# Kernel optimization log

Hardware: AMD Instinct MI355X
Metric: run time of the kernel (lower is better)

The kernel has to match this reference:

```python
import jax, jax.numpy as jnp
import numpy as np

NUM_HEADS = 8
EPS = 1e-6


def setup_inputs() -> dict:
    key = jax.random.key(0)
    k1, k2, k3 = jax.random.split(key, 3)
    B, N, C = 4, 256, 512
    x = jax.random.normal(k1, (B, N, C), dtype=jnp.float32)
    w_qkv = jax.random.normal(k2, (3 * C, C), dtype=jnp.float32) * (C ** -0.5)
    w_proj = jax.random.normal(k3, (C, C), dtype=jnp.float32) * (C ** -0.5)
    b_proj = jnp.zeros((C,), dtype=jnp.float32)
    paramR = jnp.ones((1,), dtype=jnp.float32)
    return {"x": x, "w_qkv": w_qkv, "w_proj": w_proj, "b_proj": b_proj, "paramR": paramR}


def _fourier_attention(x, w_qkv, w_proj, b_proj, paramR):
    B, N, C = x.shape
    H = NUM_HEADS
    Dh = C // H
    # qkv projection (no bias), split into per-head q,k,v: (B,H,N,Dh)
    qkv = jnp.einsum('bnc,kc->bnk', x, w_qkv).reshape(B, N, 3, H, Dh)
    q = qkv[:, :, 0].transpose(0, 2, 1, 3)
    k = qkv[:, :, 1].transpose(0, 2, 1, 3)
    v = qkv[:, :, 2].transpose(0, 2, 1, 3)
    R = paramR[0]
    # Generalized Fourier integral kernel: prod_d sin(R*(q_d - k_d))/(q_d - k_d)
    diff = q[:, :, :, None, :] - k[:, :, None, :, :]  # (B,H,Nq,Nk,Dh)
    near0 = jnp.abs(diff) < 1e-8
    safe = jnp.where(near0, jnp.float32(1.0), diff)
    s = jnp.where(near0, R, jnp.sin(R * safe) / safe)
    score = jnp.prod(s, axis=-1)  # (B,H,Nq,Nk)
    a4 = score ** 4
    attn = a4 / (jnp.sum(a4, axis=-1, keepdims=True) + EPS)  # normalize over keys
    out = jnp.einsum('bhqk,bhkd->bhqd', attn, v)
    out = out.transpose(0, 2, 1, 3).reshape(B, N, C)
    return jnp.einsum('bnc,oc->bno', out, w_proj) + b_proj


def reference(x, w_qkv, w_proj, b_proj, paramR):
    return _fourier_attention(x, w_qkv, w_proj, b_proj, paramR)
```

## Files before the change

kernel.cpp:

```cpp
#include <hip/hip_runtime.h>
#include <math.h>

#define BB 4
#define NN 256
#define CC 512
#define HH 8
#define DH 64

typedef __attribute__((ext_vector_type(8))) short bf16x8;
typedef __attribute__((ext_vector_type(4))) float f32x4;
typedef __attribute__((ext_vector_type(2))) float f32x2;

__device__ inline unsigned short f2bf(float f) {
  unsigned u = __float_as_uint(f);
  u += 0x7FFFu + ((u >> 16) & 1u);
  return (unsigned short)(u >> 16);
}
__device__ inline float bf2f(unsigned short s) {
  return __uint_as_float((unsigned)s << 16);
}

__global__ __launch_bounds__(256) void cvt_hilo3(
    const float* __restrict__ in0, unsigned short* __restrict__ h0,
    unsigned short* __restrict__ l0, const float* __restrict__ in1,
    unsigned short* __restrict__ h1, unsigned short* __restrict__ l1,
    const float* __restrict__ in2, unsigned short* __restrict__ h2,
    unsigned short* __restrict__ l2) {
  int b = blockIdx.x;
  const float* in;
  unsigned short *h, *l;
  if (b < 512) {
    in = in0; h = h0; l = l0;
  } else if (b < 1280) {
    in = in1; h = h1; l = l1; b -= 512;
  } else {
    in = in2; h = h2; l = l2; b -= 1280;
  }
  int i = (b * 256 + threadIdx.x) * 4;
  float4 f = *(const float4*)(in + i);
  float fa[4] = {f.x, f.y, f.z, f.w};
  ushort4 hv, lv;
  unsigned short* hp = (unsigned short*)&hv;
  unsigned short* lp = (unsigned short*)&lv;
#pragma unroll
  for (int j = 0; j < 4; j++) {
    unsigned short hb = f2bf(fa[j]);
    hp[j] = hb;
    lp[j] = f2bf(fa[j] - bf2f(hb));
  }
  *(ushort4*)(h + i) = hv;
  *(ushort4*)(l + i) = lv;
}

template <bool BIAS>
__global__ __launch_bounds__(256, 2) void gemm_mfma(
    const unsigned short* __restrict__ Ah, const unsigned short* __restrict__ Al,
    const unsigned short* __restrict__ Bh, const unsigned short* __restrict__ Bl,
    const float* __restrict__ bias, float* __restrict__ C, int M, int N,
    int K) {
  __shared__ unsigned short sAh[2][64][72], sAl[2][64][72];
  __shared__ unsigned short sBh[2][64][72], sBl[2][64][72];
  const int t = threadIdx.x;
  const int lane = t & 63;
  const int w = t >> 6;
  const int bm = blockIdx.y * 64;
  const int bn = blockIdx.x * 64;
  const int wr = (w >> 1) * 32;
  const int wc = (w & 1) * 32;
  const int quad = lane >> 4;
  const int l16 = lane & 15;

  const int r0 = t >> 3;
  const int r1 = r0 + 32;
  const int c8 = (t & 7) * 8;

  const size_t a0 = (size_t)(bm + r0) * K + c8;
  const size_t a1 = (size_t)(bm + r1) * K + c8;
  const size_t b0 = (size_t)(bn + r0) * K + c8;
  const size_t b1 = (size_t)(bn + r1) * K + c8;

  f32x4 acc[2][2];
#pragma unroll
  for (int i = 0; i < 2; i++)
#pragma unroll
    for (int j = 0; j < 2; j++) {
      acc[i][j][0] = 0.f;
      acc[i][j][1] = 0.f;
      acc[i][j][2] = 0.f;
      acc[i][j][3] = 0.f;
    }

  uint4 pa0, pa1, pa2, pa3, pb0, pb1, pb2, pb3;
#define GLOADS(K0)                       \
  pa0 = *(const uint4*)(Ah + a0 + (K0)); \
  pa1 = *(const uint4*)(Ah + a1 + (K0)); \
  pa2 = *(const uint4*)(Al + a0 + (K0)); \
  pa3 = *(const uint4*)(Al + a1 + (K0)); \
  pb0 = *(const uint4*)(Bh + b0 + (K0)); \
  pb1 = *(const uint4*)(Bh + b1 + (K0)); \
  pb2 = *(const uint4*)(Bl + b0 + (K0)); \
  pb3 = *(const uint4*)(Bl + b1 + (K0));

#define STORE(P)                  \
  *(uint4*)&sAh[P][r0][c8] = pa0; \
  *(uint4*)&sAh[P][r1][c8] = pa1; \
  *(uint4*)&sAl[P][r0][c8] = pa2; \
  *(uint4*)&sAl[P][r1][c8] = pa3; \
  *(uint4*)&sBh[P][r0][c8] = pb0; \
  *(uint4*)&sBh[P][r1][c8] = pb1; \
  *(uint4*)&sBl[P][r0][c8] = pb2; \
  *(uint4*)&sBl[P][r1][c8] = pb3;

  GLOADS(0)
  STORE(0)
  __syncthreads();
  GLOADS(64)

  int p = 0;
  for (int k0 = 0; k0 < K; k0 += 64) {
#pragma unroll
    for (int kk = 0; kk < 2; kk++) {
      const int kc = kk * 32 + quad * 8;
      bf16x8 ah[2], al[2], bh[2], bl[2];
#pragma unroll
      for (int i = 0; i < 2; i++) {
        ah[i] = *(const bf16x8*)&sAh[p][wr + i * 16 + l16][kc];
        al[i] = *(const bf16x8*)&sAl[p][wr + i * 16 + l16][kc];
        bh[i] = *(const bf16x8*)&sBh[p][wc + i * 16 + l16][kc];
        bl[i] = *(const bf16x8*)&sBl[p][wc + i * 16 + l16][kc];
      }
#pragma unroll
      for (int i = 0; i < 2; i++)
#pragma unroll
        for (int j = 0; j < 2; j++) {
          acc[i][j] = __builtin_amdgcn_mfma_f32_16x16x32_bf16(
              ah[i], bh[j], acc[i][j], 0, 0, 0);
          acc[i][j] = __builtin_amdgcn_mfma_f32_16x16x32_bf16(
              ah[i], bl[j], acc[i][j], 0, 0, 0);
          acc[i][j] = __builtin_amdgcn_mfma_f32_16x16x32_bf16(
              al[i], bh[j], acc[i][j], 0, 0, 0);
        }
    }
    if (k0 + 64 < K) {
      STORE(p ^ 1)
      if (k0 + 128 < K) {
        GLOADS(k0 + 128)
      }
    }
    __syncthreads();
    p ^= 1;
  }
#undef GLOADS
#undef STORE

#pragma unroll
  for (int i = 0; i < 2; i++)
#pragma unroll
    for (int j = 0; j < 2; j++) {
      int n = bn + wc + j * 16 + l16;
      float bv = BIAS ? bias[n] : 0.f;
#pragma unroll
      for (int r = 0; r < 4; r++) {
        int m = bm + wr + i * 16 + quad * 4 + r;
        C[(size_t)m * N + n] = acc[i][j][r] + bv;
      }
    }
}

__global__ __launch_bounds__(512) void fourier_attn(
    const float* __restrict__ qkv, const float* __restrict__ paramR,
    float* __restrict__ num0, float* __restrict__ num1,
    float* __restrict__ den0, float* __restrict__ den1) {
  __shared__ float Kt[64][68];
  __shared__ float Qs[16][64];
  __shared__ unsigned short Pah[16][72];
  __shared__ unsigned short Pal[16][72];
  __shared__ f32x4 Red[4][64];

  const int t = threadIdx.x;
  const int lane = t & 63;
  const int wv = t >> 6;
  const int quad = lane >> 4;
  const int l16 = lane & 15;
  const int h = blockIdx.x & 7;
  const int b = blockIdx.x >> 3;
  const int qc = blockIdx.y >> 1;
  const int kc = blockIdx.y & 1;
  const float R = paramR[0];
  const float cR = R * 0.15915494309189535f;

  const float* base = qkv + (size_t)b * NN * (3 * CC) + h * DH;

  if (t < 256) {
    int r = t >> 4;
    int c4 = (t & 15) << 2;
    *(float4*)&Qs[r][c4] =
        *(const float4*)(base + (size_t)(qc * 16 + r) * (3 * CC) + c4);
  }

  const int qi0 = wv * 2, qi1 = wv * 2 + 1;
  float Sp[2] = {0.f, 0.f};
  f32x4 oacc;
  oacc[0] = 0.f; oacc[1] = 0.f; oacc[2] = 0.f; oacc[3] = 0.f;

  const int nc = wv & 3;
  const int g2 = wv >> 2;
  const int kb = g2 * 32 + quad * 8;
  const int vcol = nc * 16 + l16;

  float4 pk[2];
#define LOADK(JT)                                                          \
  _Pragma("unroll") for (int u0 = 0; u0 < 2; u0++) {                       \
    int u = t + 512 * u0;                                                  \
    int r_ = u >> 4;                                                       \
    int c4_ = (u & 15) << 2;                                               \
    pk[u0] =                                                               \
        *(const float4*)(base + (size_t)((JT) * 64 + r_) * (3 * CC) + CC + \
                         c4_);                                             \
  }

  LOADK(kc * 2)

  const f32x2 eps2 = {1e-30f, 1e-30f};
  const f32x2 cR2 = {cR, cR};

  for (int jj = 0; jj < 2; jj++) {
    const int jt = kc * 2 + jj;
    __syncthreads();
#pragma unroll
    for (int u0 = 0; u0 < 2; u0++) {
      int u = t + 512 * u0;
      int r = u >> 4;
      int c4 = (u & 15) << 2;
      *(float4*)&Kt[r][c4] = pk[u0];
    }
    __syncthreads();
    if (jj == 0) {
      LOADK(kc * 2 + 1)
    }

    f32x2 nmA0 = {1.f, 1.f}, nmB0 = {1.f, 1.f};
    f32x2 nmA1 = {1.f, 1.f}, nmB1 = {1.f, 1.f};
    f32x2 dnA0 = {1.f, 1.f}, dnB0 = {1.f, 1.f};
    f32x2 dnA1 = {1.f, 1.f}, dnB1 = {1.f, 1.f};
#pragma unroll
    for (int d4 = 0; d4 < 16; d4++) {
      float4 k4 = *(const float4*)&Kt[lane][4 * d4];
      float4 qa = *(const float4*)&Qs[qi0][4 * d4];
      float4 qb = *(const float4*)&Qs[qi1][4 * d4];
      f32x2 kA = {k4.x, k4.y};
      f32x2 kB = {k4.z, k4.w};
      f32x2 dA0 = ((f32x2){qa.x, qa.y} - kA) + eps2;
      f32x2 dB0 = ((f32x2){qa.z, qa.w} - kB) + eps2;
      f32x2 dA1 = ((f32x2){qb.x, qb.y} - kA) + eps2;
      f32x2 dB1 = ((f32x2){qb.z, qb.w} - kB) + eps2;
      f32x2 gA0 = cR2 * dA0, gB0 = cR2 * dB0;
      f32x2 gA1 = cR2 * dA1, gB1 = cR2 * dB1;
      f32x2 sA0, sB0, sA1, sB1;
      sA0.x = __builtin_amdgcn_sinf(gA0.x);
      sA0.y = __builtin_amdgcn_sinf(gA0.y);
      sB0.x = __builtin_amdgcn_sinf(gB0.x);
      sB0.y = __builtin_amdgcn_sinf(gB0.y);
      sA1.x = __builtin_amdgcn_sinf(gA1.x);
      sA1.y = __builtin_amdgcn_sinf(gA1.y);
      sB1.x = __builtin_amdgcn_sinf(gB1.x);
      sB1.y = __builtin_amdgcn_sinf(gB1.y);
      nmA0 *= sA0;
      nmB0 *= sB0;
      nmA1 *= sA1;
      nmB1 *= sB1;
      dnA0 *= dA0;
      dnB0 *= dB0;
      dnA1 *= dA1;
      dnB1 *= dB1;
    }

    float vf[8];
#pragma unroll
    for (int j = 0; j < 8; j++) {
      vf[j] = base[(size_t)(jt * 64 + kb + j) * (3 * CC) + 2 * CC + vcol];
    }

    {
      f32x2 n0 = nmA0 * nmB0, d0 = dnA0 * dnB0;
      f32x2 n1 = nmA1 * nmB1, d1 = dnA1 * dnB1;
      float sc0 = (n0.x * n0.y) / (d0.x * d0.y);
      float sc1 = (n1.x * n1.y) / (d1.x * d1.y);
      float t0 = sc0 * sc0, t1 = sc1 * sc1;
      float a40 = t0 * t0, a41 = t1 * t1;
      Sp[0] += a40;
      Sp[1] += a41;
      unsigned short h0 = f2bf(a40), h1 = f2bf(a41);
      Pah[qi0][lane] = h0;
      Pal[qi0][lane] = f2bf(a40 - bf2f(h0));
      Pah[qi1][lane] = h1;
      Pal[qi1][lane] = f2bf(a41 - bf2f(h1));
    }
    __syncthreads();

    {
      bf16x8 pah = *(const bf16x8*)&Pah[l16][kb];
      bf16x8 pal = *(const bf16x8*)&Pal[l16][kb];
      bf16x8 vh, vl;
#pragma unroll
      for (int j = 0; j < 8; j++) {
        float f = vf[j];
        unsigned short hb = f2bf(f);
        vh[j] = (short)hb;
        vl[j] = (short)f2bf(f - bf2f(hb));
      }
      __builtin_amdgcn_s_setprio(1);
      oacc = __builtin_amdgcn_mfma_f32_16x16x32_bf16(pah, vh, oacc, 0, 0, 0);
      oacc = __builtin_amdgcn_mfma_f32_16x16x32_bf16(pah, vl, oacc, 0, 0, 0);
      oacc = __builtin_amdgcn_mfma_f32_16x16x32_bf16(pal, vh, oacc, 0, 0, 0);
      __builtin_amdgcn_s_setprio(0);
    }
  }
#undef LOADK

  float* nump = kc ? num1 : num0;
  float* denp = kc ? den1 : den0;
#pragma unroll
  for (int q = 0; q < 2; q++) {
    float s = Sp[q];
#pragma unroll
    for (int off = 32; off > 0; off >>= 1) s += __shfl_xor(s, off, 64);
    if (lane == 0) {
      int m = b * NN + qc * 16 + qi0 + q;
      denp[(size_t)m * HH + h] = s;
    }
  }
  if (wv >= 4) Red[wv - 4][lane] = oacc;
  __syncthreads();
  if (wv < 4) {
    f32x4 part = Red[wv][lane];
#pragma unroll
    for (int r = 0; r < 4; r++) {
      int q = quad * 4 + r;
      int m = b * NN + qc * 16 + q;
      nump[(size_t)m * CC + h * DH + nc * 16 + l16] = oacc[r] + part[r];
    }
  }
}

__global__ __launch_bounds__(256) void combine_norm(
    const float* __restrict__ num0, const float* __restrict__ num1,
    const float* __restrict__ den0, const float* __restrict__ den1,
    unsigned short* __restrict__ aoh, unsigned short* __restrict__ aol) {
  int e = (blockIdx.x * 256 + threadIdx.x) * 4;
  int m = e >> 9;
  int hd = (e >> 6) & 7;
  float den = den0[(size_t)m * HH + hd] + den1[(size_t)m * HH + hd] + 1e-6f;
  float4 n0 = *(const float4*)(num0 + e);
  float4 n1 = *(const float4*)(num1 + e);
  float o[4] = {(n0.x + n1.x) / den, (n0.y + n1.y) / den,
                (n0.z + n1.z) / den, (n0.w + n1.w) / den};
  ushort4 hv, lv;
  unsigned short* hp = (unsigned short*)&hv;
  unsigned short* lp = (unsigned short*)&lv;
#pragma unroll
  for (int j = 0; j < 4; j++) {
    unsigned short hb = f2bf(o[j]);
    hp[j] = hb;
    lp[j] = f2bf(o[j] - bf2f(hb));
  }
  *(ushort4*)(aoh + e) = hv;
  *(ushort4*)(aol + e) = lv;
}

extern "C" void kernel_launch(void* const* d_in, const int* in_sizes, int n_in,
                              void* d_out, int out_size, void* d_ws,
                              size_t ws_size, hipStream_t stream) {
  const float* x = (const float*)d_in[0];
  const float* w_qkv = (const float*)d_in[1];
  const float* w_proj = (const float*)d_in[2];
  const float* b_proj = (const float*)d_in[3];
  const float* paramR = (const float*)d_in[4];
  float* outp = (float*)d_out;

  const int nX = BB * NN * CC;
  const int nWq = 3 * CC * CC;
  const int nWp = CC * CC;

  unsigned short* xh = (unsigned short*)d_ws;
  unsigned short* xl = xh + nX;
  unsigned short* wqh = xl + nX;
  unsigned short* wql = wqh + nWq;
  unsigned short* wph = wql + nWq;
  unsigned short* wpl = wph + nWp;
  unsigned short* aoh = wpl + nWp;
  unsigned short* aol = aoh + nX;
  float* qkv_ws = (float*)(aol + nX);
  float* num0 = qkv_ws + 1024 * 1536;
  float* num1 = num0 + nX;
  float* den0 = num1 + nX;
  float* den1 = den0 + 1024 * HH;

  cvt_hilo3<<<1536, 256, 0, stream>>>(x, xh, xl, w_qkv, wqh, wql, w_proj, wph,
                                      wpl);

  gemm_mfma<false><<<dim3(3 * CC / 64, BB * NN / 64), 256, 0, stream>>>(
      xh, xl, wqh, wql, nullptr, qkv_ws, BB * NN, 3 * CC, CC);

  fourier_attn<<<dim3(HH * BB, (NN / 16) * 2), 512, 0, stream>>>(
      qkv_ws, paramR, num0, num1, den0, den1);

  combine_norm<<<nX / 1024, 256, 0, stream>>>(num0, num1, den0, den1, aoh,
                                              aol);

  gemm_mfma<true><<<dim3(CC / 64, BB * NN / 64), 256, 0, stream>>>(
      aoh, aol, wph, wpl, b_proj, outp, BB * NN, CC, CC);
}
```

Before: 128.5 us.

## Split attention into 4 key chunks with 8-query, 256-thread blocks

```diff
diff --git a/kernel.cpp b/kernel.cpp
--- a/kernel.cpp
+++ b/kernel.cpp
@@ -167,15 +167,16 @@
     }
 }
 
-__global__ __launch_bounds__(512) void fourier_attn(
+__global__ __launch_bounds__(256) void fourier_attn(
     const float* __restrict__ qkv, const float* __restrict__ paramR,
     float* __restrict__ num0, float* __restrict__ num1,
-    float* __restrict__ den0, float* __restrict__ den1) {
+    float* __restrict__ num2, float* __restrict__ num3,
+    float* __restrict__ den0, float* __restrict__ den1,
+    float* __restrict__ den2, float* __restrict__ den3) {
   __shared__ float Kt[64][68];
-  __shared__ float Qs[16][64];
+  __shared__ float Qs[8][64];
   __shared__ unsigned short Pah[16][72];
   __shared__ unsigned short Pal[16][72];
-  __shared__ f32x4 Red[4][64];
 
   const int t = threadIdx.x;
   const int lane = t & 63;
@@ -184,177 +185,180 @@
   const int l16 = lane & 15;
   const int h = blockIdx.x & 7;
   const int b = blockIdx.x >> 3;
-  const int qc = blockIdx.y >> 1;
-  const int kc = blockIdx.y & 1;
+  const int qg = blockIdx.y >> 2;
+  const int kc4 = blockIdx.y & 3;
   const float R = paramR[0];
   const float cR = R * 0.15915494309189535f;
 
   const float* base = qkv + (size_t)b * NN * (3 * CC) + h * DH;
-
-  if (t < 256) {
+  const int jt64 = kc4 * 64;
+
+  float4 pk[4];
+#pragma unroll
+  for (int s = 0; s < 4; s++) {
+    int u = t + 256 * s;
+    int r = u >> 4;
+    int c4 = (u & 15) << 2;
+    pk[s] = *(const float4*)(base + (size_t)(jt64 + r) * (3 * CC) + CC + c4);
+  }
+  if (t < 128) {
     int r = t >> 4;
     int c4 = (t & 15) << 2;
     *(float4*)&Qs[r][c4] =
-        *(const float4*)(base + (size_t)(qc * 16 + r) * (3 * CC) + c4);
-  }
+        *(const float4*)(base + (size_t)(qg * 8 + r) * (3 * CC) + c4);
+  }
+  if (t < 288) {
+    ((unsigned*)Pah)[288 + t] = 0u;
+    ((unsigned*)Pal)[288 + t] = 0u;
+  }
+#pragma unroll
+  for (int s = 0; s < 4; s++) {
+    int u = t + 256 * s;
+    int r = u >> 4;
+    int c4 = (u & 15) << 2;
+    *(float4*)&Kt[r][c4] = pk[s];
+  }
+  __syncthreads();
 
   const int qi0 = wv * 2, qi1 = wv * 2 + 1;
-  float Sp[2] = {0.f, 0.f};
+  const int nc = wv;
+  const int vcol = nc * 16 + l16;
+
+  const f32x2 eps2 = {1e-30f, 1e-30f};
+  const f32x2 cR2 = {cR, cR};
+  f32x2 nmA0 = {1.f, 1.f}, nmB0 = {1.f, 1.f};
+  f32x2 nmA1 = {1.f, 1.f}, nmB1 = {1.f, 1.f};
+  f32x2 dnA0 = {1.f, 1.f}, dnB0 = {1.f, 1.f};
+  f32x2 dnA1 = {1.f, 1.f}, dnB1 = {1.f, 1.f};
+#pragma unroll
+  for (int d4 = 0; d4 < 16; d4++) {
+    float4 k4 = *(const float4*)&Kt[lane][4 * d4];
+    float4 qa = *(const float4*)&Qs[qi0][4 * d4];
+    float4 qb = *(const float4*)&Qs[qi1][4 * d4];
+    f32x2 kA = {k4.x, k4.y};
+    f32x2 kB = {k4.z, k4.w};
+    f32x2 dA0 = ((f32x2){qa.x, qa.y} - kA) + eps2;
+    f32x2 dB0 = ((f32x2){qa.z, qa.w} - kB) + eps2;
+    f32x2 dA1 = ((f32x2){qb.x, qb.y} - kA) + eps2;
+    f32x2 dB1 = ((f32x2){qb.z, qb.w} - kB) + eps2;
+    f32x2 gA0 = cR2 * dA0, gB0 = cR2 * dB0;
+    f32x2 gA1 = cR2 * dA1, gB1 = cR2 * dB1;
+    f32x2 sA0, sB0, sA1, sB1;
+    sA0.x = __builtin_amdgcn_sinf(gA0.x);
+    sA0.y = __builtin_amdgcn_sinf(gA0.y);
+    sB0.x = __builtin_amdgcn_sinf(gB0.x);
+    sB0.y = __builtin_amdgcn_sinf(gB0.y);
+    sA1.x = __builtin_amdgcn_sinf(gA1.x);
+    sA1.y = __builtin_amdgcn_sinf(gA1.y);
+    sB1.x = __builtin_amdgcn_sinf(gB1.x);
+    sB1.y = __builtin_amdgcn_sinf(gB1.y);
+    nmA0 *= sA0;
+    nmB0 *= sB0;
+    nmA1 *= sA1;
+    nmB1 *= sB1;
+    dnA0 *= dA0;
+    dnB0 *= dB0;
+    dnA1 *= dA1;
+    dnB1 *= dB1;
+  }
+
+  float vfa[8], vfb[8];
+#pragma unroll
+  for (int j = 0; j < 8; j++) {
+    vfa[j] = base[(size_t)(jt64 + quad * 8 + j) * (3 * CC) + 2 * CC + vcol];
+    vfb[j] =
+        base[(size_t)(jt64 + 32 + quad * 8 + j) * (3 * CC) + 2 * CC + vcol];
+  }
+
+  float Sp[2];
+  {
+    f32x2 n0 = nmA0 * nmB0, d0 = dnA0 * dnB0;
+    f32x2 n1 = nmA1 * nmB1, d1 = dnA1 * dnB1;
+    float sc0 = (n0.x * n0.y) / (d0.x * d0.y);
+    float sc1 = (n1.x * n1.y) / (d1.x * d1.y);
+    float t0 = sc0 * sc0, t1 = sc1 * sc1;
+    float a40 = t0 * t0, a41 = t1 * t1;
+    Sp[0] = a40;
+    Sp[1] = a41;
+    unsigned short h0 = f2bf(a40), h1 = f2bf(a41);
+    Pah[qi0][lane] = h0;
+    Pal[qi0][lane] = f2bf(a40 - bf2f(h0));
+    Pah[qi1][lane] = h1;
+    Pal[qi1][lane] = f2bf(a41 - bf2f(h1));
+  }
+  __syncthreads();
+
   f32x4 oacc;
   oacc[0] = 0.f; oacc[1] = 0.f; oacc[2] = 0.f; oacc[3] = 0.f;
-
-  const int nc = wv & 3;
-  const int g2 = wv >> 2;
-  const int kb = g2 * 32 + quad * 8;
-  const int vcol = nc * 16 + l16;
-
-  float4 pk[2];
-#define LOADK(JT)                                                          \
-  _Pragma("unroll") for (int u0 = 0; u0 < 2; u0++) {                       \
-    int u = t + 512 * u0;                                                  \
-    int r_ = u >> 4;                                                       \
-    int c4_ = (u & 15) << 2;                                               \
-    pk[u0] =                                                               \
-        *(const float4*)(base + (size_t)((JT) * 64 + r_) * (3 * CC) + CC + \
-                         c4_);                                             \
-  }
-
-  LOADK(kc * 2)
-
-  const f32x2 eps2 = {1e-30f, 1e-30f};
-  const f32x2 cR2 = {cR, cR};
-
-  for (int jj = 0; jj < 2; jj++) {
-    const int jt = kc * 2 + jj;
-    __syncthreads();
-#pragma unroll
-    for (int u0 = 0; u0 < 2; u0++) {
-      int u = t + 512 * u0;
-      int r = u >> 4;
-      int c4 = (u & 15) << 2;
-      *(float4*)&Kt[r][c4] = pk[u0];
-    }
-    __syncthreads();
-    if (jj == 0) {
-      LOADK(kc * 2 + 1)
-    }
-
-    f32x2 nmA0 = {1.f, 1.f}, nmB0 = {1.f, 1.f};
-    f32x2 nmA1 = {1.f, 1.f}, nmB1 = {1.f, 1.f};
-    f32x2 dnA0 = {1.f, 1.f}, dnB0 = {1.f, 1.f};
-    f32x2 dnA1 = {1.f, 1.f}, dnB1 = {1.f, 1.f};
-#pragma unroll
-    for (int d4 = 0; d4 < 16; d4++) {
-      float4 k4 = *(const float4*)&Kt[lane][4 * d4];
-      float4 qa = *(const float4*)&Qs[qi0][4 * d4];
-      float4 qb = *(const float4*)&Qs[qi1][4 * d4];
-      f32x2 kA = {k4.x, k4.y};
-      f32x2 kB = {k4.z, k4.w};
-      f32x2 dA0 = ((f32x2){qa.x, qa.y} - kA) + eps2;
-      f32x2 dB0 = ((f32x2){qa.z, qa.w} - kB) + eps2;
-      f32x2 dA1 = ((f32x2){qb.x, qb.y} - kA) + eps2;
-      f32x2 dB1 = ((f32x2){qb.z, qb.w} - kB) + eps2;
-      f32x2 gA0 = cR2 * dA0, gB0 = cR2 * dB0;
-      f32x2 gA1 = cR2 * dA1, gB1 = cR2 * dB1;
-      f32x2 sA0, sB0, sA1, sB1;
-      sA0.x = __builtin_amdgcn_sinf(gA0.x);
-      sA0.y = __builtin_amdgcn_sinf(gA0.y);
-      sB0.x = __builtin_amdgcn_sinf(gB0.x);
-      sB0.y = __builtin_amdgcn_sinf(gB0.y);
-      sA1.x = __builtin_amdgcn_sinf(gA1.x);
-      sA1.y = __builtin_amdgcn_sinf(gA1.y);
-      sB1.x = __builtin_amdgcn_sinf(gB1.x);
-      sB1.y = __builtin_amdgcn_sinf(gB1.y);
-      nmA0 *= sA0;
-      nmB0 *= sB0;
-      nmA1 *= sA1;
-      nmB1 *= sB1;
-      dnA0 *= dA0;
-      dnB0 *= dB0;
-      dnA1 *= dA1;
-      dnB1 *= dB1;
-    }
-
-    float vf[8];
+  {
+    bf16x8 pah0 = *(const bf16x8*)&Pah[l16][quad * 8];
+    bf16x8 pal0 = *(const bf16x8*)&Pal[l16][quad * 8];
+    bf16x8 pah1 = *(const bf16x8*)&Pah[l16][32 + quad * 8];
+    bf16x8 pal1 = *(const bf16x8*)&Pal[l16][32 + quad * 8];
+    bf16x8 vh0, vl0, vh1, vl1;
 #pragma unroll
     for (int j = 0; j < 8; j++) {
-      vf[j] = base[(size_t)(jt * 64 + kb + j) * (3 * CC) + 2 * CC + vcol];
-    }
-
-    {
-      f32x2 n0 = nmA0 * nmB0, d0 = dnA0 * dnB0;
-      f32x2 n1 = nmA1 * nmB1, d1 = dnA1 * dnB1;
-      float sc0 = (n0.x * n0.y) / (d0.x * d0.y);
-      float sc1 = (n1.x * n1.y) / (d1.x * d1.y);
-      float t0 = sc0 * sc0, t1 = sc1 * sc1;
-      float a40 = t0 * t0, a41 = t1 * t1;
-      Sp[0] += a40;
-      Sp[1] += a41;
-      unsigned short h0 = f2bf(a40), h1 = f2bf(a41);
-      Pah[qi0][lane] = h0;
-      Pal[qi0][lane] = f2bf(a40 - bf2f(h0));
-      Pah[qi1][lane] = h1;
-      Pal[qi1][lane] = f2bf(a41 - bf2f(h1));
-    }
-    __syncthreads();
-
-    {
-      bf16x8 pah = *(const bf16x8*)&Pah[l16][kb];
-      bf16x8 pal = *(const bf16x8*)&Pal[l16][kb];
-      bf16x8 vh, vl;
-#pragma unroll
-      for (int j = 0; j < 8; j++) {
-        float f = vf[j];
-        unsigned short hb = f2bf(f);
-        vh[j] = (short)hb;
-        vl[j] = (short)f2bf(f - bf2f(hb));
-      }
-      __builtin_amdgcn_s_setprio(1);
-      oacc = __builtin_amdgcn_mfma_f32_16x16x32_bf16(pah, vh, oacc, 0, 0, 0);
-      oacc = __builtin_amdgcn_mfma_f32_16x16x32_bf16(pah, vl, oacc, 0, 0, 0);
-      oacc = __builtin_amdgcn_mfma_f32_16x16x32_bf16(pal, vh, oacc, 0, 0, 0);
-      __builtin_amdgcn_s_setprio(0);
-    }
-  }
-#undef LOADK
-
-  float* nump = kc ? num1 : num0;
-  float* denp = kc ? den1 : den0;
+      unsigned short hb;
+      hb = f2bf(vfa[j]);
+      vh0[j] = (short)hb;
+      vl0[j] = (short)f2bf(vfa[j] - bf2f(hb));
+      hb = f2bf(vfb[j]);
+      vh1[j] = (short)hb;
+      vl1[j] = (short)f2bf(vfb[j] - bf2f(hb));
+    }
+    __builtin_amdgcn_s_setprio(1);
+    oacc = __builtin_amdgcn_mfma_f32_16x16x32_bf16(pah0, vh0, oacc, 0, 0, 0);
+    oacc = __builtin_amdgcn_mfma_f32_16x16x32_bf16(pah0, vl0, oacc, 0, 0, 0);
+    oacc = __builtin_amdgcn_mfma_f32_16x16x32_bf16(pal0, vh0, oacc, 0, 0, 0);
+    oacc = __builtin_amdgcn_mfma_f32_16x16x32_bf16(pah1, vh1, oacc, 0, 0, 0);
+    oacc = __builtin_amdgcn_mfma_f32_16x16x32_bf16(pah1, vl1, oacc, 0, 0, 0);
+    oacc = __builtin_amdgcn_mfma_f32_16x16x32_bf16(pal1, vh1, oacc, 0, 0, 0);
+    __builtin_amdgcn_s_setprio(0);
+  }
+
+  float* nump = (kc4 == 0) ? num0 : (kc4 == 1) ? num1 : (kc4 == 2) ? num2
+                                                                   : num3;
+  float* denp = (kc4 == 0) ? den0 : (kc4 == 1) ? den1 : (kc4 == 2) ? den2
+                                                                   : den3;
 #pragma unroll
   for (int q = 0; q < 2; q++) {
     float s = Sp[q];
 #pragma unroll
     for (int off = 32; off > 0; off >>= 1) s += __shfl_xor(s, off, 64);
     if (lane == 0) {
-      int m = b * NN + qc * 16 + qi0 + q;
+      int m = b * NN + qg * 8 + qi0 + q;
       denp[(size_t)m * HH + h] = s;
     }
   }
-  if (wv >= 4) Red[wv - 4][lane] = oacc;
-  __syncthreads();
-  if (wv < 4) {
-    f32x4 part = Red[wv][lane];
-#pragma unroll
-    for (int r = 0; r < 4; r++) {
-      int q = quad * 4 + r;
-      int m = b * NN + qc * 16 + q;
-      nump[(size_t)m * CC + h * DH + nc * 16 + l16] = oacc[r] + part[r];
+#pragma unroll
+  for (int r = 0; r < 4; r++) {
+    int q = quad * 4 + r;
+    if (q < 8) {
+      int m = b * NN + qg * 8 + q;
+      nump[(size_t)m * CC + h * DH + nc * 16 + l16] = oacc[r];
     }
   }
 }
 
 __global__ __launch_bounds__(256) void combine_norm(
     const float* __restrict__ num0, const float* __restrict__ num1,
+    const float* __restrict__ num2, const float* __restrict__ num3,
     const float* __restrict__ den0, const float* __restrict__ den1,
+    const float* __restrict__ den2, const float* __restrict__ den3,
     unsigned short* __restrict__ aoh, unsigned short* __restrict__ aol) {
   int e = (blockIdx.x * 256 + threadIdx.x) * 4;
   int m = e >> 9;
   int hd = (e >> 6) & 7;
-  float den = den0[(size_t)m * HH + hd] + den1[(size_t)m * HH + hd] + 1e-6f;
+  size_t di = (size_t)m * HH + hd;
+  float den = ((den0[di] + den1[di]) + (den2[di] + den3[di])) + 1e-6f;
   float4 n0 = *(const float4*)(num0 + e);
   float4 n1 = *(const float4*)(num1 + e);
-  float o[4] = {(n0.x + n1.x) / den, (n0.y + n1.y) / den,
-                (n0.z + n1.z) / den, (n0.w + n1.w) / den};
+  float4 n2 = *(const float4*)(num2 + e);
+  float4 n3 = *(const float4*)(num3 + e);
+  float o[4] = {((n0.x + n1.x) + (n2.x + n3.x)) / den,
+                ((n0.y + n1.y) + (n2.y + n3.y)) / den,
+                ((n0.z + n1.z) + (n2.z + n3.z)) / den,
+                ((n0.w + n1.w) + (n2.w + n3.w)) / den};
   ushort4 hv, lv;
   unsigned short* hp = (unsigned short*)&hv;
   unsigned short* lp = (unsigned short*)&lv;
@@ -393,8 +397,12 @@
   float* qkv_ws = (float*)(aol + nX);
   float* num0 = qkv_ws + 1024 * 1536;
   float* num1 = num0 + nX;
-  float* den0 = num1 + nX;
+  float* num2 = num1 + nX;
+  float* num3 = num2 + nX;
+  float* den0 = num3 + nX;
   float* den1 = den0 + 1024 * HH;
+  float* den2 = den1 + 1024 * HH;
+  float* den3 = den2 + 1024 * HH;
 
   cvt_hilo3<<<1536, 256, 0, stream>>>(x, xh, xl, w_qkv, wqh, wql, w_proj, wph,
                                       wpl);
@@ -402,11 +410,11 @@
   gemm_mfma<false><<<dim3(3 * CC / 64, BB * NN / 64), 256, 0, stream>>>(
       xh, xl, wqh, wql, nullptr, qkv_ws, BB * NN, 3 * CC, CC);
 
-  fourier_attn<<<dim3(HH * BB, (NN / 16) * 2), 512, 0, stream>>>(
-      qkv_ws, paramR, num0, num1, den0, den1);
-
-  combine_norm<<<nX / 1024, 256, 0, stream>>>(num0, num1, den0, den1, aoh,
-                                              aol);
+  fourier_attn<<<dim3(HH * BB, (NN / 8) * 4), 256, 0, stream>>>(
+      qkv_ws, paramR, num0, num1, num2, num3, den0, den1, den2, den3);
+
+  combine_norm<<<nX / 1024, 256, 0, stream>>>(num0, num1, num2, num3, den0,
+                                              den1, den2, den3, aoh, aol);
 
   gemm_mfma<true><<<dim3(CC / 64, BB * NN / 64), 256, 0, stream>>>(
       aoh, aol, wph, wpl, b_proj, outp, BB * NN, CC, CC);
```

After: 124.2 us. 1.03x faster.
